# Performance work log

Measured on AMD Instinct MI355X. Metric: run time of the kernel, lower is better.

## Reference

```python
import jax, jax.numpy as jnp
import numpy as np

D_IN, D_OUT, D_K, D_V, H = 768, 768, 64, 64, 12


def setup_inputs() -> dict:
    key = jax.random.key(0)
    ks = jax.random.split(key, 16)
    b, nq, nk = 4, 1024, 1024
    inp = {
        'queries': jax.random.normal(ks[0], (b, nq, D_IN), jnp.float32),
        'keys': jax.random.normal(ks[1], (b, nk, D_IN), jnp.float32),
        'values': jax.random.normal(ks[2], (b, nk, D_IN), jnp.float32),
        'loss_map': jax.random.normal(ks[3], (b, nk, H), jnp.float32),
        'attention_mask': jax.random.randint(ks[4], (b, H, nq, nk), 0, 2).astype(bool),
        'attention_weights': jax.random.uniform(ks[5], (b, H, nq, nk), jnp.float32),
        # learned params (stored as (in, out); math-equivalent to torch Linear)
        'Wq': jax.random.normal(ks[6], (D_IN, H * D_K), jnp.float32) * 0.02,
        'bq': jnp.zeros((H * D_K,), jnp.float32),
        'Wk': jax.random.normal(ks[7], (D_IN, H * D_K), jnp.float32) * 0.02,
        'bk': jnp.zeros((H * D_K,), jnp.float32),
        'Wv': jax.random.normal(ks[8], (D_IN, H * D_V), jnp.float32) * 0.02,
        'bv': jnp.zeros((H * D_V,), jnp.float32),
        'Wo': jax.random.normal(ks[9], (H * D_V, D_OUT), jnp.float32) * 0.02,
        'bo': jnp.zeros((D_OUT,), jnp.float32),
    }
    return inp


def reference(queries, keys, values, loss_map, attention_mask, attention_weights,
              Wq, bq, Wk, bk, Wv, bv, Wo, bo):
    b, nq, _ = queries.shape
    nk = keys.shape[1]
    # projections -> (b, h, n, d)
    q = (queries @ Wq + bq).reshape(b, nq, H, D_K).transpose(0, 2, 1, 3)
    k = (keys @ Wk + bk).reshape(b, nk, H, D_K).transpose(0, 2, 1, 3)
    v = (values @ Wv + bv).reshape(b, nk, H, D_V).transpose(0, 2, 1, 3)
    # scaled scores (b, h, nq, nk)
    att = jnp.einsum('bhqd,bhkd->bhqk', q, k) / np.sqrt(D_K).astype(np.float32)
    att = att * attention_weights
    att = jnp.where(attention_mask, -jnp.inf, att)
    # additive per-key, per-head bias: loss_map (b, nk, h) -> (b, h, 1, nk)
    w_g = loss_map.transpose(0, 2, 1)[:, :, None, :]
    w_mn = jax.nn.softmax(att + w_g, axis=-1)
    # dropout is identity in eval / p=0
    out = jnp.einsum('bhqk,bhkd->bhqd', w_mn, v)
    out = out.transpose(0, 2, 1, 3).reshape(b, nq, H * D_V)
    return out @ Wo + bo
```

## Files before the change

kernel.cpp:

```cpp
#include <hip/hip_runtime.h>
#include <hip/hip_bf16.h>
#include <cmath>

static constexpr int HN = 12;
static constexpr int DHEAD = 64;
static constexpr int DMODEL = 768;
static constexpr int NQ = 1024;
static constexpr int NB = 4;
static constexpr int MROWS = NB * NQ;
static constexpr size_t PER = (size_t)NB * HN * NQ * DHEAD;
static constexpr size_t WN  = (size_t)DMODEL * DMODEL;

typedef __attribute__((ext_vector_type(8))) short bf16x8;
typedef __attribute__((ext_vector_type(4))) float f32x4;

static __device__ __forceinline__ unsigned short f2bf(float f) {
    unsigned int u = __builtin_bit_cast(unsigned int, f);
    unsigned int r = (u + 0x7FFFu + ((u >> 16) & 1u)) >> 16;
    return (unsigned short)r;
}

typedef const __attribute__((address_space(1))) unsigned int gu32;
typedef __attribute__((address_space(3))) unsigned int lu32;
static __device__ __forceinline__ void gload16(const void* g, void* l) {
    __builtin_amdgcn_global_load_lds((gu32*)g, (lu32*)l, 16, 0, 0);
}

__global__ __launch_bounds__(256)
void cvt3(const float* __restrict__ a, const float* __restrict__ b, const float* __restrict__ c,
          unsigned short* __restrict__ oa, unsigned short* __restrict__ ob, unsigned short* __restrict__ oc)
{
    const int z = blockIdx.z;
    const float* s = z == 0 ? a : z == 1 ? b : c;
    unsigned short* d = z == 0 ? oa : z == 1 ? ob : oc;
    size_t i = ((size_t)blockIdx.x * 256 + threadIdx.x) * 4;
    float4 v = *(const float4*)&s[i];
    ushort4 u;
    u.x = f2bf(v.x); u.y = f2bf(v.y); u.z = f2bf(v.z); u.w = f2bf(v.w);
    *(ushort4*)&d[i] = u;
}

__global__ __launch_bounds__(256)
void wtrans(const float* __restrict__ w0, const float* __restrict__ w1,
            const float* __restrict__ w2, const float* __restrict__ w3,
            unsigned short* __restrict__ o0, unsigned short* __restrict__ o1,
            unsigned short* __restrict__ o2, unsigned short* __restrict__ o3)
{
    const int z = blockIdx.z;
    const float* in = z == 0 ? w0 : z == 1 ? w1 : z == 2 ? w2 : w3;
    unsigned short* out = z == 0 ? o0 : z == 1 ? o1 : z == 2 ? o2 : o3;
    __shared__ float t[64][65];
    const int tid = threadIdx.x;
    const int k0 = blockIdx.x * 64, n0 = blockIdx.y * 64;
    #pragma unroll
    for (int l = 0; l < 16; ++l) {
        int idx = l * 256 + tid, r = idx >> 6, cc = idx & 63;
        t[r][cc] = in[(size_t)(k0 + r) * DMODEL + n0 + cc];
    }
    __syncthreads();
    #pragma unroll
    for (int l = 0; l < 16; ++l) {
        int idx = l * 256 + tid, r = idx >> 6, cc = idx & 63;
        out[(size_t)(n0 + r) * DMODEL + k0 + cc] = f2bf(t[cc][r]);
    }
}

static __device__ __forceinline__
void gemm_body(const unsigned short* __restrict__ A, const unsigned short* __restrict__ Wt,
               const float* __restrict__ bias, void* __restrict__ C, int layout)
{
    constexpr int K = DMODEL;
    __shared__ unsigned short As[128 * 64];
    __shared__ unsigned short Bs[128 * 64];
    const int tid = threadIdx.x, w = tid >> 6, lane = tid & 63;
    const int c = lane & 15, g = lane >> 4;
    const int wr = w >> 1, wc = w & 1;
    const int bn = blockIdx.x * 128, bm = blockIdx.y * 128;

    f32x4 acc[4][4] = {};
    for (int k0 = 0; k0 < K; k0 += 64) {
        #pragma unroll
        for (int it = 0; it < 4; ++it) {
            int idx = it * 256 + tid, r = idx >> 3, blk = idx & 7;
            int so = (blk ^ (r & 7)) << 3;
            gload16(A  + (size_t)(bm + r) * K + k0 + so, &As[(it * 256 + w * 64) * 8]);
            gload16(Wt + (size_t)(bn + r) * K + k0 + so, &Bs[(it * 256 + w * 64) * 8]);
        }
        __syncthreads();
        #pragma unroll
        for (int kk = 0; kk < 2; ++kk) {
            bf16x8 a[4], b[4];
            #pragma unroll
            for (int mi = 0; mi < 4; ++mi) {
                int row = wr * 64 + mi * 16 + c;
                a[mi] = *(const bf16x8*)&As[row * 64 + ((((kk << 2) | g) ^ (row & 7)) << 3)];
            }
            #pragma unroll
            for (int ni = 0; ni < 4; ++ni) {
                int row = wc * 64 + ni * 16 + c;
                b[ni] = *(const bf16x8*)&Bs[row * 64 + ((((kk << 2) | g) ^ (row & 7)) << 3)];
            }
            #pragma unroll
            for (int mi = 0; mi < 4; ++mi)
                #pragma unroll
                for (int ni = 0; ni < 4; ++ni)
                    acc[mi][ni] = __builtin_amdgcn_mfma_f32_16x16x32_bf16(a[mi], b[ni], acc[mi][ni], 0, 0, 0);
        }
        __syncthreads();
    }

    #pragma unroll
    for (int ni = 0; ni < 4; ++ni) {
        int col = bn + wc * 64 + ni * 16 + c;
        float bvx = bias[col];
        int hh = col >> 6, d = col & 63;
        #pragma unroll
        for (int mi = 0; mi < 4; ++mi) {
            int m0 = bm + wr * 64 + mi * 16 + 4 * g;
            int bb = m0 >> 10, nn0 = m0 & (NQ - 1);
            if (layout == 0) {
                float* o = (float*)C;
                #pragma unroll
                for (int j = 0; j < 4; ++j)
                    o[(size_t)(m0 + j) * DMODEL + col] = acc[mi][ni][j] + bvx;
            } else if (layout == 1) {
                unsigned short* o = (unsigned short*)C;
                #pragma unroll
                for (int j = 0; j < 4; ++j)
                    o[(((size_t)bb * HN + hh) * NQ + nn0 + j) * DHEAD + d] =
                        f2bf(acc[mi][ni][j] + bvx);
            } else {
                unsigned short* o = (unsigned short*)C;
                ushort4 u;
                u.x = f2bf(acc[mi][ni][0] + bvx);
                u.y = f2bf(acc[mi][ni][1] + bvx);
                u.z = f2bf(acc[mi][ni][2] + bvx);
                u.w = f2bf(acc[mi][ni][3] + bvx);
                *(ushort4*)&o[(((size_t)bb * HN + hh) * DHEAD + d) * NQ + nn0] = u;
            }
        }
    }
}

__global__ __launch_bounds__(256)
void qkv_gemm(const unsigned short* __restrict__ qa, const unsigned short* __restrict__ ka,
              const unsigned short* __restrict__ va,
              const unsigned short* __restrict__ wq, const unsigned short* __restrict__ wk,
              const unsigned short* __restrict__ wv,
              const float* __restrict__ bq, const float* __restrict__ bk, const float* __restrict__ bv,
              unsigned short* __restrict__ qo, unsigned short* __restrict__ ko,
              unsigned short* __restrict__ vo)
{
    const int z = blockIdx.z;
    const unsigned short* A  = z == 0 ? qa : z == 1 ? ka : va;
    const unsigned short* Wt = z == 0 ? wq : z == 1 ? wk : wv;
    const float* bias        = z == 0 ? bq : z == 1 ? bk : bv;
    unsigned short* C        = z == 0 ? qo : z == 1 ? ko : vo;
    gemm_body(A, Wt, bias, C, z == 2 ? 2 : 1);
}

__global__ __launch_bounds__(256)
void o_gemm(const unsigned short* __restrict__ A, const unsigned short* __restrict__ Wt,
            const float* __restrict__ bias, float* __restrict__ C)
{
    gemm_body(A, Wt, bias, C, 0);
}

__global__ __launch_bounds__(256)
void attn_mfma(const unsigned short* __restrict__ qws,
               const unsigned short* __restrict__ kws,
               const unsigned short* __restrict__ vtws,
               const float* __restrict__ aw, const int* __restrict__ mask,
               const float* __restrict__ lm, unsigned short* __restrict__ out)
{
    const int qt = blockIdx.x, h = blockIdx.y, b = blockIdx.z;
    const int tid = threadIdx.x;
    const int w = tid >> 6, lane = tid & 63;
    const int c = lane & 15, g = lane >> 4;

    __shared__ unsigned short Qs[64 * 64];
    __shared__ unsigned short Ks[2][64 * 64];
    __shared__ unsigned short Vs[2][64 * 64];
    __shared__ unsigned short Ps[4][16 * 64];
    __shared__ float lms[NQ];

    const size_t bh = (size_t)b * HN + h;
    const unsigned short* qbase = qws + (bh * NQ + (size_t)qt * 64) * DHEAD;
    const unsigned short* kbase = kws + bh * NQ * DHEAD;
    const unsigned short* vtbase = vtws + bh * DHEAD * NQ;

    #pragma unroll
    for (int it = 0; it < 2; ++it) {
        int idx = it * 256 + tid, r = idx >> 3, blk = idx & 7;
        gload16(qbase + (size_t)r * DHEAD + ((blk ^ (r & 7)) << 3),
                &Qs[(it * 256 + w * 64) * 8]);
    }
    #pragma unroll
    for (int it = 0; it < 4; ++it) {
        int key = it * 256 + tid;
        lms[key] = lm[((size_t)b * NQ + key) * HN + h];
    }

    size_t awrow[4];
    #pragma unroll
    for (int j = 0; j < 4; ++j)
        awrow[j] = (bh * NQ + (size_t)(qt * 64 + w * 16 + 4 * g + j)) * (size_t)NQ;

    auto stageKV = [&](int kt, int bufi) {
        const int k0 = kt * 64;
        #pragma unroll
        for (int it = 0; it < 2; ++it) {
            int idx = it * 256 + tid, r = idx >> 3, blk = idx & 7;
            int so = (blk ^ (r & 7)) << 3;
            gload16(kbase + (size_t)(k0 + r) * DHEAD + so, &Ks[bufi][(it * 256 + w * 64) * 8]);
            gload16(vtbase + (size_t)r * NQ + k0 + so,     &Vs[bufi][(it * 256 + w * 64) * 8]);
        }
    };

    float awv[4][4]; int mkv[4][4];
    #pragma unroll
    for (int nt = 0; nt < 4; ++nt)
        #pragma unroll
        for (int j = 0; j < 4; ++j) {
            size_t idx = awrow[j] + nt * 16 + c;
            awv[nt][j] = aw[idx];
            mkv[nt][j] = mask[idx];
        }
    stageKV(0, 0);
    __syncthreads();

    const int qrow = w * 16 + c;
    const bf16x8 qf0 = *(const bf16x8*)&Qs[qrow * 64 + ((g ^ (c & 7)) << 3)];
    const bf16x8 qf1 = *(const bf16x8*)&Qs[qrow * 64 + (((g | 4) ^ (c & 7)) << 3)];

    f32x4 O[4] = {{0,0,0,0},{0,0,0,0},{0,0,0,0},{0,0,0,0}};
    float mrun[4], lrun[4];
    #pragma unroll
    for (int j = 0; j < 4; ++j) { mrun[j] = -1e30f; lrun[j] = 0.f; }

    #pragma unroll 2
    for (int kt = 0; kt < 16; ++kt) {
        const int cur = kt & 1;
        const int k0 = kt * 64;
        float awn[4][4]; int mkn[4][4];
        if (kt < 15) {
            stageKV(kt + 1, cur ^ 1);
            #pragma unroll
            for (int nt = 0; nt < 4; ++nt)
                #pragma unroll
                for (int j = 0; j < 4; ++j) {
                    size_t idx = awrow[j] + (kt + 1) * 64 + nt * 16 + c;
                    awn[nt][j] = aw[idx];
                    mkn[nt][j] = mask[idx];
                }
        }
        const unsigned short* ksb = &Ks[cur][0];
        const unsigned short* vsb = &Vs[cur][0];

        f32x4 s[4] = {{0,0,0,0},{0,0,0,0},{0,0,0,0},{0,0,0,0}};
        #pragma unroll
        for (int kk = 0; kk < 2; ++kk) {
            bf16x8 qf = kk ? qf1 : qf0;
            #pragma unroll
            for (int nt = 0; nt < 4; ++nt) {
                int krow = nt * 16 + c;
                bf16x8 kf = *(const bf16x8*)&ksb[krow * 64 + ((((kk << 2) | g) ^ (c & 7)) << 3)];
                s[nt] = __builtin_amdgcn_mfma_f32_16x16x32_bf16(qf, kf, s[nt], 0, 0, 0);
            }
        }

        float p[4][4], tmax[4];
        #pragma unroll
        for (int j = 0; j < 4; ++j) tmax[j] = -INFINITY;
        #pragma unroll
        for (int nt = 0; nt < 4; ++nt) {
            float lmv = lms[k0 + nt * 16 + c];
            #pragma unroll
            for (int j = 0; j < 4; ++j) {
                float v = s[nt][j] * 0.125f * awv[nt][j];
                v = mkv[nt][j] ? -INFINITY : v;
                v += lmv;
                p[nt][j] = v;
                tmax[j] = fmaxf(tmax[j], v);
            }
        }
        #pragma unroll
        for (int off = 1; off < 16; off <<= 1)
            #pragma unroll
            for (int j = 0; j < 4; ++j)
                tmax[j] = fmaxf(tmax[j], __shfl_xor(tmax[j], off));

        float mn[4], scal[4], rs[4];
        #pragma unroll
        for (int j = 0; j < 4; ++j) {
            mn[j] = fmaxf(mrun[j], tmax[j]);
            scal[j] = __expf(mrun[j] - mn[j]);
            mrun[j] = mn[j];
            rs[j] = 0.f;
        }
        #pragma unroll
        for (int nt = 0; nt < 4; ++nt)
            #pragma unroll
            for (int j = 0; j < 4; ++j) {
                float e = __expf(p[nt][j] - mn[j]);
                p[nt][j] = e;
                rs[j] += e;
            }
        #pragma unroll
        for (int off = 1; off < 16; off <<= 1)
            #pragma unroll
            for (int j = 0; j < 4; ++j)
                rs[j] += __shfl_xor(rs[j], off);
        #pragma unroll
        for (int j = 0; j < 4; ++j) lrun[j] = lrun[j] * scal[j] + rs[j];
        #pragma unroll
        for (int nd = 0; nd < 4; ++nd)
            #pragma unroll
            for (int j = 0; j < 4; ++j) O[nd][j] *= scal[j];

        unsigned short* pw = &Ps[w][0];
        #pragma unroll
        for (int nt = 0; nt < 4; ++nt)
            #pragma unroll
            for (int j = 0; j < 4; ++j) {
                int row = 4 * g + j, col = nt * 16 + c;
                pw[row * 64 + (((col >> 3) ^ (row & 7)) << 3) + (col & 7)] = f2bf(p[nt][j]);
            }
        #pragma unroll
        for (int kk = 0; kk < 2; ++kk) {
            bf16x8 pa = *(const bf16x8*)&pw[c * 64 + ((((kk << 2) | g) ^ (c & 7)) << 3)];
            #pragma unroll
            for (int nd = 0; nd < 4; ++nd) {
                int vrow = nd * 16 + c;
                bf16x8 vf = *(const bf16x8*)&vsb[vrow * 64 + ((((kk << 2) | g) ^ (c & 7)) << 3)];
                O[nd] = __builtin_amdgcn_mfma_f32_16x16x32_bf16(pa, vf, O[nd], 0, 0, 0);
            }
        }
        __syncthreads();
        if (kt < 15) {
            #pragma unroll
            for (int nt = 0; nt < 4; ++nt)
                #pragma unroll
                for (int j = 0; j < 4; ++j) { awv[nt][j] = awn[nt][j]; mkv[nt][j] = mkn[nt][j]; }
        }
    }

    #pragma unroll
    for (int j = 0; j < 4; ++j) {
        float inv = 1.f / lrun[j];
        int qglob = qt * 64 + w * 16 + 4 * g + j;
        size_t ob = ((size_t)b * NQ + qglob) * DMODEL + h * DHEAD;
        #pragma unroll
        for (int nd = 0; nd < 4; ++nd)
            out[ob + nd * 16 + c] = f2bf(O[nd][j] * inv);
    }
}

extern "C" void kernel_launch(void* const* d_in, const int* in_sizes, int n_in,
                              void* d_out, int out_size, void* d_ws, size_t ws_size,
                              hipStream_t stream)
{
    const float* queries = (const float*)d_in[0];
    const float* keys    = (const float*)d_in[1];
    const float* values  = (const float*)d_in[2];
    const float* lossmap = (const float*)d_in[3];
    const int*   mask    = (const int*)d_in[4];
    const float* aw      = (const float*)d_in[5];
    const float* Wq = (const float*)d_in[6];
    const float* bq = (const float*)d_in[7];
    const float* Wk = (const float*)d_in[8];
    const float* bk = (const float*)d_in[9];
    const float* Wv = (const float*)d_in[10];
    const float* bv = (const float*)d_in[11];
    const float* Wo = (const float*)d_in[12];
    const float* bo = (const float*)d_in[13];

    unsigned short* p = (unsigned short*)d_ws;
    unsigned short* qbf  = p; p += PER;
    unsigned short* kbf  = p; p += PER;
    unsigned short* vbf  = p; p += PER;
    unsigned short* qws  = p; p += PER;
    unsigned short* kws  = p; p += PER;
    unsigned short* vtws = p; p += PER;
    unsigned short* aobf = p; p += PER;
    unsigned short* wqt  = p; p += WN;
    unsigned short* wkt  = p; p += WN;
    unsigned short* wvt  = p; p += WN;
    unsigned short* wot  = p; p += WN;

    cvt3<<<dim3((unsigned)(PER / 1024), 1, 3), 256, 0, stream>>>(queries, keys, values, qbf, kbf, vbf);
    wtrans<<<dim3(12, 12, 4), 256, 0, stream>>>(Wq, Wk, Wv, Wo, wqt, wkt, wvt, wot);
    qkv_gemm<<<dim3(DMODEL / 128, MROWS / 128, 3), 256, 0, stream>>>(
        qbf, kbf, vbf, wqt, wkt, wvt, bq, bk, bv, qws, kws, vtws);
    attn_mfma<<<dim3(NQ / 64, HN, NB), 256, 0, stream>>>(qws, kws, vtws, aw, mask, lossmap, aobf);
    o_gemm<<<dim3(DMODEL / 128, MROWS / 128), 256, 0, stream>>>(aobf, wot, bo, (float*)d_out);
}
```

Before: 197.7 us.

## Read Q/K/V fragments directly from global memory and fold mask/scale into FMA

Drops the LDS staging and double buffering of Q, K and V tiles in the attention kernel. Each wave now loads its MFMA fragments straight from global memory, which also removes the per-iteration block barrier. The attention weight, scale, mask and loss bias are precomputed during prefetch into a multiplier and an additive term, so each score costs one FMA. This saves LDS traffic and synchronisation, but the four waves of a block now load the same K/V tiles separately from global/L2, and direct loads may stall the MFMAs. Masked entries now use -1e30 instead of -inf.

```diff
diff --git a/kernel.cpp b/kernel.cpp
--- a/kernel.cpp
+++ b/kernel.cpp
@@ -178,9 +178,6 @@
     const int w = tid >> 6, lane = tid & 63;
     const int c = lane & 15, g = lane >> 4;
 
-    __shared__ unsigned short Qs[64 * 64];
-    __shared__ unsigned short Ks[2][64 * 64];
-    __shared__ unsigned short Vs[2][64 * 64];
     __shared__ unsigned short Ps[4][16 * 64];
     __shared__ float lms[NQ];
 
@@ -190,72 +187,51 @@
     const unsigned short* vtbase = vtws + bh * DHEAD * NQ;
 
     #pragma unroll
-    for (int it = 0; it < 2; ++it) {
-        int idx = it * 256 + tid, r = idx >> 3, blk = idx & 7;
-        gload16(qbase + (size_t)r * DHEAD + ((blk ^ (r & 7)) << 3),
-                &Qs[(it * 256 + w * 64) * 8]);
-    }
-    #pragma unroll
     for (int it = 0; it < 4; ++it) {
         int key = it * 256 + tid;
         lms[key] = lm[((size_t)b * NQ + key) * HN + h];
     }
+    __syncthreads();
+
+    const int qrow = w * 16 + c;
+    const bf16x8 qf0 = *(const bf16x8*)&qbase[qrow * DHEAD + g * 8];
+    const bf16x8 qf1 = *(const bf16x8*)&qbase[qrow * DHEAD + 32 + g * 8];
 
     size_t awrow[4];
     #pragma unroll
     for (int j = 0; j < 4; ++j)
         awrow[j] = (bh * NQ + (size_t)(qt * 64 + w * 16 + 4 * g + j)) * (size_t)NQ;
 
-    auto stageKV = [&](int kt, int bufi) {
+    float scv[4][4], bsv[4][4];
+    auto prefetch = [&](int kt, float sc[4][4], float bs[4][4]) {
         const int k0 = kt * 64;
         #pragma unroll
-        for (int it = 0; it < 2; ++it) {
-            int idx = it * 256 + tid, r = idx >> 3, blk = idx & 7;
-            int so = (blk ^ (r & 7)) << 3;
-            gload16(kbase + (size_t)(k0 + r) * DHEAD + so, &Ks[bufi][(it * 256 + w * 64) * 8]);
-            gload16(vtbase + (size_t)r * NQ + k0 + so,     &Vs[bufi][(it * 256 + w * 64) * 8]);
+        for (int nt = 0; nt < 4; ++nt) {
+            float lmv = lms[k0 + nt * 16 + c];
+            #pragma unroll
+            for (int j = 0; j < 4; ++j) {
+                size_t idx = awrow[j] + k0 + nt * 16 + c;
+                float a = aw[idx];
+                int m = mask[idx];
+                sc[nt][j] = m ? 0.f : 0.125f * a;
+                bs[nt][j] = m ? -1e30f : lmv;
+            }
         }
     };
-
-    float awv[4][4]; int mkv[4][4];
-    #pragma unroll
-    for (int nt = 0; nt < 4; ++nt)
-        #pragma unroll
-        for (int j = 0; j < 4; ++j) {
-            size_t idx = awrow[j] + nt * 16 + c;
-            awv[nt][j] = aw[idx];
-            mkv[nt][j] = mask[idx];
-        }
-    stageKV(0, 0);
-    __syncthreads();
-
-    const int qrow = w * 16 + c;
-    const bf16x8 qf0 = *(const bf16x8*)&Qs[qrow * 64 + ((g ^ (c & 7)) << 3)];
-    const bf16x8 qf1 = *(const bf16x8*)&Qs[qrow * 64 + (((g | 4) ^ (c & 7)) << 3)];
+    prefetch(0, scv, bsv);
 
     f32x4 O[4] = {{0,0,0,0},{0,0,0,0},{0,0,0,0},{0,0,0,0}};
     float mrun[4], lrun[4];
     #pragma unroll
     for (int j = 0; j < 4; ++j) { mrun[j] = -1e30f; lrun[j] = 0.f; }
 
+    unsigned short* pw = &Ps[w][0];
+
     #pragma unroll 2
     for (int kt = 0; kt < 16; ++kt) {
-        const int cur = kt & 1;
         const int k0 = kt * 64;
-        float awn[4][4]; int mkn[4][4];
-        if (kt < 15) {
-            stageKV(kt + 1, cur ^ 1);
-            #pragma unroll
-            for (int nt = 0; nt < 4; ++nt)
-                #pragma unroll
-                for (int j = 0; j < 4; ++j) {
-                    size_t idx = awrow[j] + (kt + 1) * 64 + nt * 16 + c;
-                    awn[nt][j] = aw[idx];
-                    mkn[nt][j] = mask[idx];
-                }
-        }
-        const unsigned short* ksb = &Ks[cur][0];
-        const unsigned short* vsb = &Vs[cur][0];
+        float scn[4][4], bsn[4][4];
+        if (kt < 15) prefetch(kt + 1, scn, bsn);
 
         f32x4 s[4] = {{0,0,0,0},{0,0,0,0},{0,0,0,0},{0,0,0,0}};
         #pragma unroll
@@ -263,8 +239,7 @@
             bf16x8 qf = kk ? qf1 : qf0;
             #pragma unroll
             for (int nt = 0; nt < 4; ++nt) {
-                int krow = nt * 16 + c;
-                bf16x8 kf = *(const bf16x8*)&ksb[krow * 64 + ((((kk << 2) | g) ^ (c & 7)) << 3)];
+                bf16x8 kf = *(const bf16x8*)&kbase[(size_t)(k0 + nt * 16 + c) * DHEAD + kk * 32 + g * 8];
                 s[nt] = __builtin_amdgcn_mfma_f32_16x16x32_bf16(qf, kf, s[nt], 0, 0, 0);
             }
         }
@@ -273,17 +248,13 @@
         #pragma unroll
         for (int j = 0; j < 4; ++j) tmax[j] = -INFINITY;
         #pragma unroll
-        for (int nt = 0; nt < 4; ++nt) {
-            float lmv = lms[k0 + nt * 16 + c];
+        for (int nt = 0; nt < 4; ++nt)
             #pragma unroll
             for (int j = 0; j < 4; ++j) {
-                float v = s[nt][j] * 0.125f * awv[nt][j];
-                v = mkv[nt][j] ? -INFINITY : v;
-                v += lmv;
+                float v = fmaf(s[nt][j], scv[nt][j], bsv[nt][j]);
                 p[nt][j] = v;
                 tmax[j] = fmaxf(tmax[j], v);
             }
-        }
         #pragma unroll
         for (int off = 1; off < 16; off <<= 1)
             #pragma unroll
@@ -318,7 +289,6 @@
             #pragma unroll
             for (int j = 0; j < 4; ++j) O[nd][j] *= scal[j];
 
-        unsigned short* pw = &Ps[w][0];
         #pragma unroll
         for (int nt = 0; nt < 4; ++nt)
             #pragma unroll
@@ -331,17 +301,15 @@
             bf16x8 pa = *(const bf16x8*)&pw[c * 64 + ((((kk << 2) | g) ^ (c & 7)) << 3)];
             #pragma unroll
             for (int nd = 0; nd < 4; ++nd) {
-                int vrow = nd * 16 + c;
-                bf16x8 vf = *(const bf16x8*)&vsb[vrow * 64 + ((((kk << 2) | g) ^ (c & 7)) << 3)];
+                bf16x8 vf = *(const bf16x8*)&vtbase[(size_t)(nd * 16 + c) * NQ + k0 + kk * 32 + g * 8];
                 O[nd] = __builtin_amdgcn_mfma_f32_16x16x32_bf16(pa, vf, O[nd], 0, 0, 0);
             }
         }
-        __syncthreads();
         if (kt < 15) {
             #pragma unroll
             for (int nt = 0; nt < 4; ++nt)
                 #pragma unroll
-                for (int j = 0; j < 4; ++j) { awv[nt][j] = awn[nt][j]; mkv[nt][j] = mkn[nt][j]; }
+                for (int j = 0; j < 4; ++j) { scv[nt][j] = scn[nt][j]; bsv[nt][j] = bsn[nt][j]; }
         }
     }
 
```

Result: slower. 245.1 us (+24.0%).
